# Kernel tuning notes

Measured on AMD Instinct MI355X. Metric: run time of the kernel, lower is better.

The kernel has to match this reference:

```python
import jax, jax.numpy as jnp
import numpy as np

VOL_LO = np.array([-40.0, -40.0, -1.0], np.float32)
VOL_HI = np.array([40.0, 40.0, 5.4], np.float32)
VOXEL = 0.4
GRID = (200, 200, 16)  # ((hi-lo)/voxel).int() as in __init__
NUM_CLASSES = 18
EMPTY_LABEL = 17
K = 10  # static per-gaussian tile: 6*sigma_max/VOXEL + 1 <= 10 since sigma <= 0.5
EPS = 1e-6
N_GAUSS = 8192


def quat_to_rotmat(q):
    # wxyz quaternion -> rotation matrix (normalized, as in 3DGS)
    q = q / jnp.linalg.norm(q, axis=-1, keepdims=True)
    w, x, y, z = q[..., 0], q[..., 1], q[..., 2], q[..., 3]
    R = jnp.stack([
        1 - 2 * (y * y + z * z), 2 * (x * y - w * z), 2 * (x * z + w * y),
        2 * (x * y + w * z), 1 - 2 * (x * x + z * z), 2 * (y * z - w * x),
        2 * (x * z - w * y), 2 * (y * z + w * x), 1 - 2 * (x * x + y * y),
    ], axis=-1)
    return R.reshape(q.shape[:-1] + (3, 3))


def _grid_coords():
    H, W, D = GRID
    ii, jj, kk = jnp.meshgrid(jnp.arange(H), jnp.arange(W), jnp.arange(D), indexing='ij')
    g = jnp.stack([ii, jj, kk], axis=-1).astype(jnp.float32) + 0.5  # voxel centers
    return g * VOXEL + jnp.asarray(VOL_LO)


def setup_inputs() -> dict:
    key = jax.random.key(0)
    k1, k2, k3, k4, k5 = jax.random.split(key, 5)
    lo = jnp.asarray(VOL_LO)
    hi = jnp.asarray(VOL_HI)
    means3d = jax.random.uniform(k1, (N_GAUSS, 3)) * (hi - lo) + lo
    opacities = jax.random.uniform(k2, (N_GAUSS, 1))
    features = jax.random.normal(k3, (N_GAUSS, NUM_CLASSES - 1))
    scales = jax.random.uniform(k4, (N_GAUSS, 3)) * 0.4 + 0.1  # sigma in [0.1, 0.5]
    rotations = jax.random.normal(k5, (N_GAUSS, 4))
    empty_scalar = jnp.full((1,), 10.0, jnp.float32)
    return {"means3d": means3d, "opacities": opacities, "features": features,
            "scales": scales, "rotations": rotations, "empty_scalar": empty_scalar}


def reference(means3d, opacities, features, scales, rotations, empty_scalar):
    H, W, D = GRID
    lo = jnp.asarray(VOL_LO)
    hi = jnp.asarray(VOL_HI)
    dims = jnp.array(GRID, jnp.int32)

    # covariances = (R diag(s)) (R diag(s))^T
    R = quat_to_rotmat(rotations)                 # [N,3,3]
    Lm = R * scales[:, None, :]
    cov = Lm @ jnp.swapaxes(Lm, -1, -2)           # [N,3,3]
    cov_inv = jnp.linalg.inv(cov)
    sig = jnp.sqrt(jnp.diagonal(cov, axis1=-2, axis2=-1))  # [N,3]

    # clamped 3-sigma bounds + skip test (strict, matching torch)
    b_lo = jnp.clip(means3d - 3.0 * sig, lo, hi)
    b_hi = jnp.clip(means3d + 3.0 * sig, lo, hi)
    valid = (((b_lo > lo) | (b_hi > lo)) & ((b_lo < hi) | (b_hi < hi))).all(-1)  # [N]
    i_lo = ((b_lo - lo) / VOXEL).astype(jnp.int32)
    i_hi = ((b_hi - lo) / VOXEL).astype(jnp.int32)

    # static KxKxK tile per gaussian, masked to the inclusive [i_lo, i_hi] slice
    o = jnp.arange(K, dtype=jnp.int32)
    oi, oj, ok = jnp.meshgrid(o, o, o, indexing='ij')
    offs = jnp.stack([oi, oj, ok], -1).reshape(-1, 3)          # [K3,3]
    vox = i_lo[:, None, :] + offs[None]                        # [N,K3,3]
    mask = (vox <= i_hi[:, None, :]).all(-1) & (vox < dims).all(-1) & valid[:, None]

    coords = (vox.astype(jnp.float32) + 0.5) * VOXEL + lo      # voxel centers
    diff = coords - means3d[:, None, :]                        # [N,K3,3]
    maha = jnp.einsum('nki,nij,nkj->nk', diff, cov_inv, diff)  # [N,K3]
    dens = jnp.where(mask, opacities * jnp.exp(-0.5 * maha), 0.0)

    flat = jnp.where(mask, vox[..., 0] * (W * D) + vox[..., 1] * D + vox[..., 2], 0)

    feat18 = jnp.concatenate([features, jnp.zeros_like(features[:, :1])], -1)  # [N,18]
    gd = jnp.zeros((H * W * D,), jnp.float32).at[flat.reshape(-1)].add(dens.reshape(-1))
    gf = jnp.zeros((H * W * D, NUM_CLASSES), jnp.float32).at[flat.reshape(-1)].add(
        (dens[..., None] * feat18[:, None, :]).reshape(-1, NUM_CLASSES))

    # appended 'empty' gaussian spans the full grid -> splat densely
    gc = _grid_coords()                                        # [H,W,D,3]
    e_mean = (lo + hi) / 2.0
    e_range = hi - lo
    e_inv = jnp.diag(1.0 / (e_range ** 2))
    de = gc - e_mean
    maha_e = jnp.einsum('hwdi,ij,hwdj->hwd', de, e_inv, de)
    dens_e = jnp.exp(-0.5 * maha_e)                            # empty opacity = 1
    e_feat = jnp.zeros((NUM_CLASSES,), jnp.float32).at[EMPTY_LABEL].add(empty_scalar[0])

    grid_density = gd.reshape(H, W, D) + dens_e
    grid_feats = gf.reshape(H, W, D, NUM_CLASSES) + dens_e[..., None] * e_feat
    grid_feats = grid_feats / jnp.maximum(grid_density[..., None], EPS)
    return grid_density[..., None], grid_feats
```

## Files before the change

### kernel.cpp

```cpp
#include <hip/hip_runtime.h>

namespace {
constexpr int GH = 200, GW = 200, GD = 16;
constexpr int NV = GH * GW * GD;
constexpr int NCLS = 18;
constexpr int NF = 17;
constexpr int NG = 8192;
constexpr int KMAX = 10;
constexpr float VOX = 0.4f;
constexpr float LO0 = -40.f, LO1 = -40.f, LO2 = -1.f;
constexpr float HI0 = 40.f, HI1 = 40.f, HI2 = 5.4f;
constexpr float EPSV = 1e-6f;

constexpr int TILE_XY = 4;
constexpr int NTX = GH / TILE_XY;
constexpr int NTY = GW / TILE_XY;
constexpr int NT = NTX * NTY;
constexpr int REC_DW = 32;
constexpr int CAP = 1024;
}

__global__ __launch_bounds__(256) void gv_bin(
    const float* __restrict__ means,
    const float* __restrict__ opac,
    const float* __restrict__ feats,
    const float* __restrict__ scales,
    const float* __restrict__ rots,
    int4* __restrict__ boxes,
    float* __restrict__ recs,
    int* __restrict__ counts,
    int* __restrict__ lists)
{
    const int g = blockIdx.x * blockDim.x + threadIdx.x;
    if (g >= NG) return;

    const float mx = means[g * 3 + 0];
    const float my = means[g * 3 + 1];
    const float mz = means[g * 3 + 2];
    const float sx = scales[g * 3 + 0];
    const float sy = scales[g * 3 + 1];
    const float sz = scales[g * 3 + 2];
    float qw = rots[g * 4 + 0];
    float qx = rots[g * 4 + 1];
    float qy = rots[g * 4 + 2];
    float qz = rots[g * 4 + 3];

    const float qn = rsqrtf(qw * qw + qx * qx + qy * qy + qz * qz);
    qw *= qn; qx *= qn; qy *= qn; qz *= qn;
    const float r00 = 1.f - 2.f * (qy * qy + qz * qz);
    const float r01 = 2.f * (qx * qy - qw * qz);
    const float r02 = 2.f * (qx * qz + qw * qy);
    const float r10 = 2.f * (qx * qy + qw * qz);
    const float r11 = 1.f - 2.f * (qx * qx + qz * qz);
    const float r12 = 2.f * (qy * qz - qw * qx);
    const float r20 = 2.f * (qx * qz - qw * qy);
    const float r21 = 2.f * (qy * qz + qw * qx);
    const float r22 = 1.f - 2.f * (qx * qx + qy * qy);

    const float s0 = sx * sx, s1 = sy * sy, s2 = sz * sz;
    const float c00 = r00 * r00 * s0 + r01 * r01 * s1 + r02 * r02 * s2;
    const float c11 = r10 * r10 * s0 + r11 * r11 * s1 + r12 * r12 * s2;
    const float c22 = r20 * r20 * s0 + r21 * r21 * s1 + r22 * r22 * s2;
    const float i0 = 1.f / s0, i1 = 1.f / s1, i2 = 1.f / s2;
    const float a00 = r00 * r00 * i0 + r01 * r01 * i1 + r02 * r02 * i2;
    const float a01 = r00 * r10 * i0 + r01 * r11 * i1 + r02 * r12 * i2;
    const float a02 = r00 * r20 * i0 + r01 * r21 * i1 + r02 * r22 * i2;
    const float a11 = r10 * r10 * i0 + r11 * r11 * i1 + r12 * r12 * i2;
    const float a12 = r10 * r20 * i0 + r11 * r21 * i1 + r12 * r22 * i2;
    const float a22 = r20 * r20 * i0 + r21 * r21 * i1 + r22 * r22 * i2;

    const float m3[3] = { mx, my, mz };
    const float sg[3] = { sqrtf(c00), sqrtf(c11), sqrtf(c22) };
    const float lo3[3] = { LO0, LO1, LO2 };
    const float hi3[3] = { HI0, HI1, HI2 };
    const int dims[3] = { GH, GW, GD };

    int il[3], sp[3];
    bool valid = true;
#pragma unroll
    for (int ax = 0; ax < 3; ++ax) {
        const float bl = fminf(fmaxf(m3[ax] - 3.f * sg[ax], lo3[ax]), hi3[ax]);
        const float bh = fminf(fmaxf(m3[ax] + 3.f * sg[ax], lo3[ax]), hi3[ax]);
        valid = valid &&
                (((bl > lo3[ax]) || (bh > lo3[ax])) && ((bl < hi3[ax]) || (bh < hi3[ax])));
        const int a = (int)((bl - lo3[ax]) / VOX);
        const int b = (int)((bh - lo3[ax]) / VOX);
        int s = b - a + 1;
        s = min(s, KMAX);
        s = min(s, dims[ax] - a);
        s = max(s, 0);
        il[ax] = a;
        sp[ax] = s;
    }

    boxes[g] = make_int4(il[0], il[1], il[2], sp[0] | (sp[1] << 8) | (sp[2] << 16));

    float* R = recs + (size_t)g * REC_DW;
    R[0] = mx; R[1] = my; R[2] = mz; R[3] = opac[g];
    R[4] = a00; R[5] = a01; R[6] = a02; R[7] = a11; R[8] = a12; R[9] = a22;
#pragma unroll
    for (int c = 0; c < NF; ++c) R[10 + c] = feats[g * NF + c];

    if (!valid || sp[0] <= 0 || sp[1] <= 0 || sp[2] <= 0) return;

    const int tx0 = il[0] / TILE_XY;
    const int tx1 = (il[0] + sp[0] - 1) / TILE_XY;
    const int ty0 = il[1] / TILE_XY;
    const int ty1 = (il[1] + sp[1] - 1) / TILE_XY;
    for (int tx = tx0; tx <= tx1; ++tx)
        for (int ty = ty0; ty <= ty1; ++ty) {
            const int tile = tx * NTY + ty;
            const int idx = atomicAdd(counts + tile, 1);
            if (idx < CAP) lists[(size_t)tile * CAP + idx] = g;
        }
}

__global__ __launch_bounds__(256) void gv_gather(
    const int4* __restrict__ boxes,
    const float* __restrict__ recs,
    const int* __restrict__ counts,
    const int* __restrict__ lists,
    const float* __restrict__ empty_scalar,
    float* __restrict__ out)
{
    const int tile = blockIdx.x;
    const int tx = tile / NTY;
    const int ty = tile - tx * NTY;
    const int X0 = tx * TILE_XY;
    const int Y0 = ty * TILE_XY;

    const int t = threadIdx.x;
    const int lz = t & 15;
    const int ly = (t >> 4) & 3;
    const int lx = t >> 6;
    const int vx = X0 + lx;
    const int vy = Y0 + ly;
    const int vz = lz;
    const float cx = ((float)vx + 0.5f) * VOX + LO0;
    const float cy = ((float)vy + 0.5f) * VOX + LO1;
    const float cz = ((float)vz + 0.5f) * VOX + LO2;

    const int n = min(counts[tile], CAP);
    const int* __restrict__ lst = lists + (size_t)tile * CAP;

    float accd = 0.f;
    float accf[NF];
#pragma unroll
    for (int c = 0; c < NF; ++c) accf[c] = 0.f;

    int g1 = 0;
    int4 b1 = make_int4(0, 0, 0, 0);
    float p1[10];
#pragma unroll
    for (int u = 0; u < 10; ++u) p1[u] = 0.f;
    if (n > 0) {
        g1 = __builtin_amdgcn_readfirstlane(lst[0]);
        b1 = boxes[g1];
        const float* R = recs + (size_t)g1 * REC_DW;
#pragma unroll
        for (int u = 0; u < 10; ++u) p1[u] = R[u];
    }

    for (int i = 0; i < n; ++i) {
        const int g0 = g1;
        const int4 b0 = b1;
        float p0[10];
#pragma unroll
        for (int u = 0; u < 10; ++u) p0[u] = p1[u];
        const float* __restrict__ F0 = recs + (size_t)g0 * REC_DW + 10;
        float f0[NF];
#pragma unroll
        for (int c = 0; c < NF; ++c) f0[c] = F0[c];

        if (i + 1 < n) {
            g1 = __builtin_amdgcn_readfirstlane(lst[i + 1]);
            b1 = boxes[g1];
            const float* R = recs + (size_t)g1 * REC_DW;
#pragma unroll
            for (int u = 0; u < 10; ++u) p1[u] = R[u];
        }

        const bool in =
            ((unsigned)(vx - b0.x) < (unsigned)(b0.w & 255)) &
            ((unsigned)(vy - b0.y) < (unsigned)((b0.w >> 8) & 255)) &
            ((unsigned)(vz - b0.z) < (unsigned)((b0.w >> 16) & 255));

        const float dx = cx - p0[0];
        const float dy = cy - p0[1];
        const float dz = cz - p0[2];
        const float maha = p0[4] * dx * dx + p0[7] * dy * dy + p0[9] * dz * dz
                         + 2.f * (p0[5] * dx * dy + p0[6] * dx * dz + p0[8] * dy * dz);
        const float dens = p0[3] * __expf(-0.5f * maha);

        if (in) {
            accd += dens;
#pragma unroll
            for (int c = 0; c < NF; ++c) accf[c] += dens * f0[c];
        }
    }

    const float ex = (cx - 0.5f * (LO0 + HI0)) / (HI0 - LO0);
    const float ey = (cy - 0.5f * (LO1 + HI1)) / (HI1 - LO1);
    const float ez = (cz - 0.5f * (LO2 + HI2)) / (HI2 - LO2);
    const float dens_e = __expf(-0.5f * (ex * ex + ey * ey + ez * ez));

    const float density = accd + dens_e;
    const int v = (vx * GW + vy) * GD + vz;
    out[v] = density;

    const float inv = 1.f / fmaxf(density, EPSV);
    float* of = out + NV + (size_t)v * NCLS;
#pragma unroll
    for (int c = 0; c < NF; ++c) of[c] = accf[c] * inv;
    of[NF] = dens_e * empty_scalar[0] * inv;
}

extern "C" void kernel_launch(void* const* d_in, const int* in_sizes, int n_in,
                              void* d_out, int out_size, void* d_ws, size_t ws_size,
                              hipStream_t stream) {
    const float* means  = (const float*)d_in[0];
    const float* opac   = (const float*)d_in[1];
    const float* feats  = (const float*)d_in[2];
    const float* scales = (const float*)d_in[3];
    const float* rots   = (const float*)d_in[4];
    const float* esc    = (const float*)d_in[5];

    int4*  boxes  = (int4*)d_ws;
    float* recs   = (float*)(boxes + NG);
    int*   counts = (int*)(recs + (size_t)NG * REC_DW);
    int*   lists  = counts + ((NT + 63) & ~63);

    hipMemsetAsync(counts, 0, sizeof(int) * ((NT + 63) & ~63), stream);

    gv_bin<<<NG / 256, 256, 0, stream>>>(means, opac, feats, scales, rots,
                                         boxes, recs, counts, lists);
    gv_gather<<<NT, 256, 0, stream>>>(boxes, recs, counts, lists, esc, (float*)d_out);
}
```

Baseline: 113.1 us.

## Gather with one wave per tile, four z-voxels per thread

```diff
diff --git a/kernel.cpp b/kernel.cpp
--- a/kernel.cpp
+++ b/kernel.cpp
@@ -115,7 +115,7 @@
         }
 }
 
-__global__ __launch_bounds__(256) void gv_gather(
+__global__ __launch_bounds__(64) void gv_gather(
     const int4* __restrict__ boxes,
     const float* __restrict__ recs,
     const int* __restrict__ counts,
@@ -126,93 +126,107 @@
     const int tile = blockIdx.x;
     const int tx = tile / NTY;
     const int ty = tile - tx * NTY;
-    const int X0 = tx * TILE_XY;
-    const int Y0 = ty * TILE_XY;
-
-    const int t = threadIdx.x;
-    const int lz = t & 15;
-    const int ly = (t >> 4) & 3;
-    const int lx = t >> 6;
-    const int vx = X0 + lx;
-    const int vy = Y0 + ly;
-    const int vz = lz;
+
+    const int lane = threadIdx.x;
+    const int lx = lane >> 4;
+    const int ly = (lane >> 2) & 3;
+    const int vz0 = (lane & 3) << 2;
+
+    const int vx = tx * TILE_XY + lx;
+    const int vy = ty * TILE_XY + ly;
     const float cx = ((float)vx + 0.5f) * VOX + LO0;
     const float cy = ((float)vy + 0.5f) * VOX + LO1;
-    const float cz = ((float)vz + 0.5f) * VOX + LO2;
 
     const int n = min(counts[tile], CAP);
     const int* __restrict__ lst = lists + (size_t)tile * CAP;
 
-    float accd = 0.f;
-    float accf[NF];
-#pragma unroll
-    for (int c = 0; c < NF; ++c) accf[c] = 0.f;
-
-    int g1 = 0;
+    float accd[4] = { 0.f, 0.f, 0.f, 0.f };
+    float accf[4][NF];
+#pragma unroll
+    for (int j = 0; j < 4; ++j)
+#pragma unroll
+        for (int c = 0; c < NF; ++c) accf[j][c] = 0.f;
+
     int4 b1 = make_int4(0, 0, 0, 0);
-    float p1[10];
-#pragma unroll
-    for (int u = 0; u < 10; ++u) p1[u] = 0.f;
+    float P1[27];
+#pragma unroll
+    for (int u = 0; u < 27; ++u) P1[u] = 0.f;
     if (n > 0) {
-        g1 = __builtin_amdgcn_readfirstlane(lst[0]);
-        b1 = boxes[g1];
-        const float* R = recs + (size_t)g1 * REC_DW;
-#pragma unroll
-        for (int u = 0; u < 10; ++u) p1[u] = R[u];
+        const int g = __builtin_amdgcn_readfirstlane(lst[0]);
+        b1 = boxes[g];
+        const float* R = recs + (size_t)g * REC_DW;
+#pragma unroll
+        for (int u = 0; u < 27; ++u) P1[u] = R[u];
     }
 
     for (int i = 0; i < n; ++i) {
-        const int g0 = g1;
         const int4 b0 = b1;
-        float p0[10];
-#pragma unroll
-        for (int u = 0; u < 10; ++u) p0[u] = p1[u];
-        const float* __restrict__ F0 = recs + (size_t)g0 * REC_DW + 10;
-        float f0[NF];
-#pragma unroll
-        for (int c = 0; c < NF; ++c) f0[c] = F0[c];
+        float P0[27];
+#pragma unroll
+        for (int u = 0; u < 27; ++u) P0[u] = P1[u];
 
         if (i + 1 < n) {
-            g1 = __builtin_amdgcn_readfirstlane(lst[i + 1]);
-            b1 = boxes[g1];
-            const float* R = recs + (size_t)g1 * REC_DW;
-#pragma unroll
-            for (int u = 0; u < 10; ++u) p1[u] = R[u];
+            const int g = __builtin_amdgcn_readfirstlane(lst[i + 1]);
+            b1 = boxes[g];
+            const float* R = recs + (size_t)g * REC_DW;
+#pragma unroll
+            for (int u = 0; u < 27; ++u) P1[u] = R[u];
         }
 
-        const bool in =
+        const bool inxy =
             ((unsigned)(vx - b0.x) < (unsigned)(b0.w & 255)) &
-            ((unsigned)(vy - b0.y) < (unsigned)((b0.w >> 8) & 255)) &
-            ((unsigned)(vz - b0.z) < (unsigned)((b0.w >> 16) & 255));
-
-        const float dx = cx - p0[0];
-        const float dy = cy - p0[1];
-        const float dz = cz - p0[2];
-        const float maha = p0[4] * dx * dx + p0[7] * dy * dy + p0[9] * dz * dz
-                         + 2.f * (p0[5] * dx * dy + p0[6] * dx * dz + p0[8] * dy * dz);
-        const float dens = p0[3] * __expf(-0.5f * maha);
-
-        if (in) {
-            accd += dens;
-#pragma unroll
-            for (int c = 0; c < NF; ++c) accf[c] += dens * f0[c];
+            ((unsigned)(vy - b0.y) < (unsigned)((b0.w >> 8) & 255));
+        const unsigned spz = (unsigned)((b0.w >> 16) & 255);
+
+        const float dx = cx - P0[0];
+        const float dy = cy - P0[1];
+        const float q0 = P0[4] * dx * dx + P0[7] * dy * dy + 2.f * P0[5] * dx * dy;
+        const float q1 = 2.f * (P0[6] * dx + P0[8] * dy);
+
+#pragma unroll
+        for (int j = 0; j < 4; ++j) {
+            const float cz = ((float)(vz0 + j) + 0.5f) * VOX + LO2;
+            const float dz = cz - P0[2];
+            const float maha = q0 + dz * (q1 + P0[9] * dz);
+            const bool in = inxy & ((unsigned)(vz0 + j - b0.z) < spz);
+            const float dens = P0[3] * __expf(-0.5f * maha);
+            if (in) {
+                accd[j] += dens;
+#pragma unroll
+                for (int c = 0; c < NF; ++c) accf[j][c] += dens * P0[10 + c];
+            }
         }
     }
 
+    const float es = empty_scalar[0];
     const float ex = (cx - 0.5f * (LO0 + HI0)) / (HI0 - LO0);
     const float ey = (cy - 0.5f * (LO1 + HI1)) / (HI1 - LO1);
-    const float ez = (cz - 0.5f * (LO2 + HI2)) / (HI2 - LO2);
-    const float dens_e = __expf(-0.5f * (ex * ex + ey * ey + ez * ez));
-
-    const float density = accd + dens_e;
-    const int v = (vx * GW + vy) * GD + vz;
-    out[v] = density;
-
-    const float inv = 1.f / fmaxf(density, EPSV);
-    float* of = out + NV + (size_t)v * NCLS;
-#pragma unroll
-    for (int c = 0; c < NF; ++c) of[c] = accf[c] * inv;
-    of[NF] = dens_e * empty_scalar[0] * inv;
+    const float exy = ex * ex + ey * ey;
+
+    float dsv[4], dev[4];
+#pragma unroll
+    for (int j = 0; j < 4; ++j) {
+        const float cz = ((float)(vz0 + j) + 0.5f) * VOX + LO2;
+        const float ez = (cz - 0.5f * (LO2 + HI2)) / (HI2 - LO2);
+        dev[j] = __expf(-0.5f * (exy + ez * ez));
+        dsv[j] = accd[j] + dev[j];
+    }
+
+    const int vbase = (vx * GW + vy) * GD + vz0;
+    *(float4*)(out + vbase) = make_float4(dsv[0], dsv[1], dsv[2], dsv[3]);
+
+#pragma unroll
+    for (int j = 0; j < 4; ++j) {
+        const float inv = 1.f / fmaxf(dsv[j], EPSV);
+        float vals[NCLS];
+#pragma unroll
+        for (int c = 0; c < NF; ++c) vals[c] = accf[j][c] * inv;
+        vals[NF] = dev[j] * es * inv;
+        float2* of2 = (float2*)(out + NV + (size_t)(vbase + j) * NCLS);
+#pragma unroll
+        for (int p = 0; p < NCLS / 2; ++p)
+            of2[p] = make_float2(vals[2 * p], vals[2 * p + 1]);
+    }
 }
 
 extern "C" void kernel_launch(void* const* d_in, const int* in_sizes, int n_in,
@@ -234,5 +248,5 @@
 
     gv_bin<<<NG / 256, 256, 0, stream>>>(means, opac, feats, scales, rots,
                                          boxes, recs, counts, lists);
-    gv_gather<<<NT, 256, 0, stream>>>(boxes, recs, counts, lists, esc, (float*)d_out);
-}
+    gv_gather<<<NT, 64, 0, stream>>>(boxes, recs, counts, lists, esc, (float*)d_out);
+}
```

After: 108.3 us. 1.04x faster.
